# Kernel optimization log

Hardware: AMD Instinct MI355X
Metric: run time of the kernel (lower is better)

The kernel has to match this reference:

```python
import jax, jax.numpy as jnp
import numpy as np
import math

B, D_MODEL, EMB, ORDER, SEQ = 4, 64, 33, 64, 256
TARGET, FAST_PCT, SLOW_PCT = 0.01, 0.3, 1.5


def _pos_emb(L, emb_dim):
    # PositionalEmbedding: t in [0,1], complex exponential bands
    t = jnp.linspace(0.0, 1.0, L)[None, :, None]                     # [1,L,1]
    bands = (emb_dim - 1) // 2
    t_r = jnp.linspace(0.0, L - 1.0, L)[None, :, None]
    w = 2.0 * math.pi * t_r / L
    f = jnp.linspace(1e-4, bands - 1.0, bands)[None, None]
    zc = jnp.exp(-1j * f * w)
    z = jnp.concatenate([t, zc.real, zc.imag], axis=-1)              # [1,L,emb_dim]
    return z.astype(jnp.float32), t.astype(jnp.float32)


def setup_inputs() -> dict:
    key = jax.random.key(0)
    ks = jax.random.split(key, 24)
    z, _ = _pos_emb(SEQ, EMB)

    def lin(k, fan_in, fan_out):
        return jax.random.normal(k, (fan_in, fan_out), jnp.float32) / np.sqrt(fan_in)

    inp = {
        'x': jax.random.normal(ks[0], (B, D_MODEL, SEQ, SEQ), jnp.float32),
        'z': z,
        'Xw1': lin(ks[1], EMB, ORDER), 'Xb1': jax.random.normal(ks[2], (ORDER,), jnp.float32) * 0.02,
        'Xw2': lin(ks[3], ORDER, ORDER), 'Xb2': jax.random.normal(ks[4], (ORDER,), jnp.float32) * 0.02,
        'Xw3': lin(ks[5], ORDER, ORDER), 'Xb3': jax.random.normal(ks[6], (ORDER,), jnp.float32) * 0.02,
        'Xwo': lin(ks[7], ORDER, D_MODEL),
        'Xfreq': jnp.ones((1, ORDER), jnp.float32),  # Sin freq, w=1, shared across layers
        'Yw1': lin(ks[8], EMB, ORDER), 'Yb1': jax.random.normal(ks[9], (ORDER,), jnp.float32) * 0.02,
        'Yw2': lin(ks[10], ORDER, ORDER), 'Yb2': jax.random.normal(ks[11], (ORDER,), jnp.float32) * 0.02,
        'Yw3': lin(ks[12], ORDER, ORDER), 'Yb3': jax.random.normal(ks[13], (ORDER,), jnp.float32) * 0.02,
        'Ywo': lin(ks[14], ORDER, D_MODEL),
        'Yfreq': jnp.ones((1, ORDER), jnp.float32),
        'bias': jax.random.normal(ks[15], (D_MODEL,), jnp.float32),
        'L': SEQ,
    }
    return inp


def _implicit_filter(z, w1, b1, w2, b2, w3, b3, wo, freq, t, deltas):
    # MLP with shared Sin activation, then exponential modulation (shift=0)
    h = jnp.sin(freq * (z @ w1 + b1))
    h = jnp.sin(freq * (h @ w2 + b2))
    h = jnp.sin(freq * (h @ w3 + b3))
    h = h @ wo                                   # [1,L,d_model]
    decay = jnp.exp(-t * jnp.abs(deltas))        # [1,L,d_model]
    return h * decay


def reference(x, z, Xw1, Xb1, Xw2, Xb2, Xw3, Xb3, Xwo, Xfreq,
              Yw1, Yb1, Yw2, Yb2, Yw3, Yb3, Ywo, Yfreq, bias, L):
    d_model = x.shape[1]
    t = jnp.linspace(0.0, 1.0, L)[None, :, None].astype(jnp.float32)
    max_dec = math.log(TARGET) / FAST_PCT
    min_dec = math.log(TARGET) / SLOW_PCT
    deltas = jnp.linspace(min_dec, max_dec, d_model)[None, None].astype(jnp.float32)

    hx = _implicit_filter(z, Xw1, Xb1, Xw2, Xb2, Xw3, Xb3, Xwo, Xfreq, t, deltas)
    hy = _implicit_filter(z, Yw1, Yb1, Yw2, Yb2, Yw3, Yb3, Ywo, Yfreq, t, deltas)
    # separable outer-product 2D kernel: [1,L,L,d_model] -> [d_model,L,L]
    k = jnp.einsum('ijk,imk->ijmk', hx, hy)[0]
    k = jnp.transpose(k, (2, 0, 1))

    fft_size = 2 * L
    k_f = jnp.fft.rfft2(k, s=(fft_size, fft_size)) / fft_size       # [D, 2L, L+1]
    u_f = jnp.fft.rfft2(x.astype(jnp.float32), s=(fft_size, fft_size))  # [B, D, 2L, L+1]
    y = jnp.fft.irfft2(u_f * k_f, s=(fft_size, fft_size))[..., :L, :L]
    out = y + x * bias[:, None, None]
    return out.astype(x.dtype)
```

## Files before the change

### kernel.cpp

```cpp
#include <hip/hip_runtime.h>

#define SL 256

typedef _Float16 f16;
typedef _Float16 f16x8 __attribute__((ext_vector_type(8)));
typedef _Float16 f16x4 __attribute__((ext_vector_type(4)));
typedef float f32x4 __attribute__((ext_vector_type(4)));

__global__ __launch_bounds__(64) void k_filters(
    const float* __restrict__ z,
    const float* __restrict__ Xw1, const float* __restrict__ Xb1,
    const float* __restrict__ Xw2, const float* __restrict__ Xb2,
    const float* __restrict__ Xw3, const float* __restrict__ Xb3,
    const float* __restrict__ Xwo, const float* __restrict__ Xfreq,
    const float* __restrict__ Yw1, const float* __restrict__ Yb1,
    const float* __restrict__ Yw2, const float* __restrict__ Yb2,
    const float* __restrict__ Yw3, const float* __restrict__ Yb3,
    const float* __restrict__ Ywo, const float* __restrict__ Yfreq,
    f16* __restrict__ hxT, f16* __restrict__ hyT)
{
    const int l = blockIdx.x;
    const int sel = blockIdx.y;
    const int t = threadIdx.x;
    const float* w1 = sel ? Yw1 : Xw1;  const float* b1 = sel ? Yb1 : Xb1;
    const float* w2 = sel ? Yw2 : Xw2;  const float* b2 = sel ? Yb2 : Xb2;
    const float* w3 = sel ? Yw3 : Xw3;  const float* b3 = sel ? Yb3 : Xb3;
    const float* wo = sel ? Ywo : Xwo;  const float* freq = sel ? Yfreq : Xfreq;
    f16* hT = sel ? hyT : hxT;

    __shared__ float zb[33];
    __shared__ float ha[64];
    __shared__ float hb[64];

    if (t < 33) zb[t] = z[l * 33 + t];
    __syncthreads();

    const float fr = freq[t];
    float s = b1[t];
    for (int k = 0; k < 33; ++k) s += zb[k] * w1[k * 64 + t];
    ha[t] = sinf(fr * s);
    __syncthreads();

    s = b2[t];
    for (int k = 0; k < 64; ++k) s += ha[k] * w2[k * 64 + t];
    hb[t] = sinf(fr * s);
    __syncthreads();

    s = b3[t];
    for (int k = 0; k < 64; ++k) s += hb[k] * w3[k * 64 + t];
    ha[t] = sinf(fr * s);
    __syncthreads();

    s = 0.f;
    for (int k = 0; k < 64; ++k) s += ha[k] * wo[k * 64 + t];

    const float MIN_DEC = -3.0701134573253937f;
    const float MAX_DEC = -15.350567286626968f;
    float ad = fabsf(MIN_DEC + (MAX_DEC - MIN_DEC) * ((float)t / 63.0f));
    float tl = (float)l / 255.0f;
    hT[t * 256 + l] = (f16)(s * expf(-tl * ad));
}

__device__ __forceinline__ f16x8 cvt8(float4 a, float4 b)
{
    f16x8 h;
    h[0] = (f16)a.x; h[1] = (f16)a.y; h[2] = (f16)a.z; h[3] = (f16)a.w;
    h[4] = (f16)b.x; h[5] = (f16)b.y; h[6] = (f16)b.z; h[7] = (f16)b.w;
    return h;
}

__device__ __forceinline__ void build_R(f16* R, const f16* __restrict__ hc,
                                        int tid)
{
    for (int idx = tid; idx < 8 * 520; idx += 512) {
        int c = idx / 520;
        int k = idx - c * 520;
        int u = k + c;
        R[idx] = (u <= 255) ? hc[255 - u] : (f16)0.f;
    }
}

template<int J0>
__device__ __forceinline__ void phase1(
    const float* __restrict__ xr0, const float* __restrict__ xr1,
    const f16* __restrict__ R, f32x4 (&acc)[16], int ln, int quad)
{
    constexpr int QS = (J0 == 0) ? 4 : 8;
    float4 a0 = *(const float4*)xr0;
    float4 a1 = *(const float4*)(xr0 + 4);
    float4 b0 = *(const float4*)xr1;
    float4 b1 = *(const float4*)(xr1 + 4);

#pragma unroll
    for (int s = 0; s < QS; ++s) {
        const int q0 = s * 32;
        f16x8 af0 = cvt8(a0, a1);
        f16x8 af1 = cvt8(b0, b1);
        if (s + 1 < QS) {
            a0 = *(const float4*)(xr0 + q0 + 32);
            a1 = *(const float4*)(xr0 + q0 + 36);
            b0 = *(const float4*)(xr1 + q0 + 32);
            b1 = *(const float4*)(xr1 + q0 + 36);
        }
#pragma unroll
        for (int c8 = 0; c8 < 8; ++c8) {
            if (32 * s <= J0 + c8 * 16 + 15) {
                int j = J0 + c8 * 16 + ln;
                int s0 = 255 - j + q0 + quad * 8;
                int c = s0 & 7;
                f16x8 bf = *(const f16x8*)&R[c * 520 + (s0 - c)];
                acc[c8] = __builtin_amdgcn_mfma_f32_16x16x32_f16(
                    af0, bf, acc[c8], 0, 0, 0);
                acc[8 + c8] = __builtin_amdgcn_mfma_f32_16x16x32_f16(
                    af1, bf, acc[8 + c8], 0, 0, 0);
            }
        }
    }
}

__global__ __launch_bounds__(512, 4) void k_fused(
    const float* __restrict__ x, const f16* __restrict__ hxT,
    const f16* __restrict__ hyT, const float* __restrict__ bias,
    float* __restrict__ out)
{
    const int bd = blockIdx.x & 255;
    const int j0 = (blockIdx.x >> 8) << 7;
    const int d  = bd & 63;
    const int tid  = threadIdx.x;
    const int lane = tid & 63;
    const int wave = tid >> 6;
    const int ln   = lane & 15;
    const int quad = lane >> 4;

    __shared__ __align__(16) f16 tmp[128 * 256];
    __shared__ __align__(16) f16 R[8 * 520];

    const float* xbd = x + (size_t)bd * (SL * SL);

    build_R(R, hyT + d * 256, tid);

    f32x4 acc[16];
#pragma unroll
    for (int a = 0; a < 16; ++a) acc[a] = (f32x4){0.f, 0.f, 0.f, 0.f};

    __syncthreads();

    {
        const float* xr0 = xbd + (wave * 32 + ln) * SL + quad * 8;
        const float* xr1 = xr0 + 16 * SL;
        if (j0 == 0) phase1<0>(xr0, xr1, R, acc, ln, quad);
        else         phase1<128>(xr0, xr1, R, acc, ln, quad);

#pragma unroll
        for (int r = 0; r < 2; ++r)
#pragma unroll
            for (int c8 = 0; c8 < 8; ++c8) {
                int jl = c8 * 16 + ln;
                int pb = wave * 32 + r * 16 + quad * 4;
                f32x4 a = acc[r * 8 + c8];
                f16x4 v;
                v[0] = (f16)a[0]; v[1] = (f16)a[1];
                v[2] = (f16)a[2]; v[3] = (f16)a[3];
                *(f16x4*)&tmp[jl * 256 + (pb ^ ((jl & 7) << 3))] = v;
            }
    }

    __syncthreads();
    build_R(R, hxT + d * 256, tid);
#pragma unroll
    for (int a = 0; a < 16; ++a) acc[a] = (f32x4){0.f, 0.f, 0.f, 0.f};
    __syncthreads();

    const int igrp = wave & 3;
    const int jgrp = wave >> 2;
    const int nst = (igrp + 1) * 2;
    for (int s = 0; s < nst; ++s) {
        const int p0 = s * 32;
        f16x8 af[4];
#pragma unroll
        for (int rt = 0; rt < 4; ++rt) {
            int jl = jgrp * 64 + rt * 16 + ln;
            int off = (p0 + quad * 8) ^ ((jl & 7) << 3);
            af[rt] = *(const f16x8*)&tmp[jl * 256 + off];
        }
#pragma unroll
        for (int ct = 0; ct < 4; ++ct) {
            if (p0 <= igrp * 64 + ct * 16 + 15) {
                int i = igrp * 64 + ct * 16 + ln;
                int s0 = 255 - i + p0 + quad * 8;
                int c = s0 & 7;
                f16x8 bf = *(const f16x8*)&R[c * 520 + (s0 - c)];
#pragma unroll
                for (int rt = 0; rt < 4; ++rt)
                    acc[rt * 4 + ct] = __builtin_amdgcn_mfma_f32_16x16x32_f16(
                        af[rt], bf, acc[rt * 4 + ct], 0, 0, 0);
            }
        }
    }

    const float bv = bias[d];
    const float sc = 1.0f / 512.0f;
    float* obd = out + (size_t)bd * (SL * SL);
#pragma unroll
    for (int rt = 0; rt < 4; ++rt)
#pragma unroll
        for (int ct = 0; ct < 4; ++ct) {
            int i = igrp * 64 + ct * 16 + ln;
            int j = j0 + jgrp * 64 + rt * 16 + quad * 4;
            f32x4 a = acc[rt * 4 + ct];
            float4 xv = *(const float4*)(xbd + i * SL + j);
            float4 o;
            o.x = a[0] * sc + xv.x * bv;
            o.y = a[1] * sc + xv.y * bv;
            o.z = a[2] * sc + xv.z * bv;
            o.w = a[3] * sc + xv.w * bv;
            *(float4*)(obd + i * SL + j) = o;
        }
}

extern "C" void kernel_launch(void* const* d_in, const int* in_sizes, int n_in,
                              void* d_out, int out_size, void* d_ws, size_t ws_size,
                              hipStream_t stream)
{
    (void)in_sizes; (void)n_in; (void)out_size; (void)ws_size;
    const float* x     = (const float*)d_in[0];
    const float* z     = (const float*)d_in[1];
    const float* Xw1   = (const float*)d_in[2];
    const float* Xb1   = (const float*)d_in[3];
    const float* Xw2   = (const float*)d_in[4];
    const float* Xb2   = (const float*)d_in[5];
    const float* Xw3   = (const float*)d_in[6];
    const float* Xb3   = (const float*)d_in[7];
    const float* Xwo   = (const float*)d_in[8];
    const float* Xfreq = (const float*)d_in[9];
    const float* Yw1   = (const float*)d_in[10];
    const float* Yb1   = (const float*)d_in[11];
    const float* Yw2   = (const float*)d_in[12];
    const float* Yb2   = (const float*)d_in[13];
    const float* Yw3   = (const float*)d_in[14];
    const float* Yb3   = (const float*)d_in[15];
    const float* Ywo   = (const float*)d_in[16];
    const float* Yfreq = (const float*)d_in[17];
    const float* bias  = (const float*)d_in[18];

    f16* hxT = (f16*)d_ws;
    f16* hyT = hxT + 64 * 256;

    k_filters<<<dim3(256, 2), 64, 0, stream>>>(
        z, Xw1, Xb1, Xw2, Xb2, Xw3, Xb3, Xwo, Xfreq,
        Yw1, Yb1, Yw2, Yb2, Yw3, Yb3, Ywo, Yfreq, hxT, hyT);
    k_fused<<<512, 512, 0, stream>>>(x, hxT, hyT, bias, (float*)d_out);
}
```

Measured before the change: 169.8 us.

## Balance triangular causal-conv work across blocks and waves via interleaved tile mapping

```diff
diff --git a/kernel.cpp b/kernel.cpp
--- a/kernel.cpp
+++ b/kernel.cpp
@@ -80,12 +80,18 @@
     }
 }
 
-template<int J0>
+template<int H>
+__device__ __forceinline__ constexpr int jmap(int c8)
+{
+    return H ? 64 + c8 * 16 : (c8 < 4 ? c8 * 16 : 192 + (c8 - 4) * 16);
+}
+
+template<int H>
 __device__ __forceinline__ void phase1(
     const float* __restrict__ xr0, const float* __restrict__ xr1,
     const f16* __restrict__ R, f32x4 (&acc)[16], int ln, int quad)
 {
-    constexpr int QS = (J0 == 0) ? 4 : 8;
+    constexpr int QS = H ? 6 : 8;
     float4 a0 = *(const float4*)xr0;
     float4 a1 = *(const float4*)(xr0 + 4);
     float4 b0 = *(const float4*)xr1;
@@ -104,8 +110,8 @@
         }
 #pragma unroll
         for (int c8 = 0; c8 < 8; ++c8) {
-            if (32 * s <= J0 + c8 * 16 + 15) {
-                int j = J0 + c8 * 16 + ln;
+            if (32 * s <= jmap<H>(c8) + 15) {
+                int j = jmap<H>(c8) + ln;
                 int s0 = 255 - j + q0 + quad * 8;
                 int c = s0 & 7;
                 f16x8 bf = *(const f16x8*)&R[c * 520 + (s0 - c)];
@@ -124,7 +130,7 @@
     float* __restrict__ out)
 {
     const int bd = blockIdx.x & 255;
-    const int j0 = (blockIdx.x >> 8) << 7;
+    const int h  = blockIdx.x >> 8;
     const int d  = bd & 63;
     const int tid  = threadIdx.x;
     const int lane = tid & 63;
@@ -148,8 +154,8 @@
     {
         const float* xr0 = xbd + (wave * 32 + ln) * SL + quad * 8;
         const float* xr1 = xr0 + 16 * SL;
-        if (j0 == 0) phase1<0>(xr0, xr1, R, acc, ln, quad);
-        else         phase1<128>(xr0, xr1, R, acc, ln, quad);
+        if (h == 0) phase1<0>(xr0, xr1, R, acc, ln, quad);
+        else        phase1<1>(xr0, xr1, R, acc, ln, quad);
 
 #pragma unroll
         for (int r = 0; r < 2; ++r)
@@ -173,7 +179,7 @@
 
     const int igrp = wave & 3;
     const int jgrp = wave >> 2;
-    const int nst = (igrp + 1) * 2;
+    const int nst = ((192 + igrp * 16 + 15) >> 5) + 1;
     for (int s = 0; s < nst; ++s) {
         const int p0 = s * 32;
         f16x8 af[4];
@@ -185,8 +191,8 @@
         }
 #pragma unroll
         for (int ct = 0; ct < 4; ++ct) {
-            if (p0 <= igrp * 64 + ct * 16 + 15) {
-                int i = igrp * 64 + ct * 16 + ln;
+            if (p0 <= ct * 64 + igrp * 16 + 15) {
+                int i = ct * 64 + igrp * 16 + ln;
                 int s0 = 255 - i + p0 + quad * 8;
                 int c = s0 & 7;
                 f16x8 bf = *(const f16x8*)&R[c * 520 + (s0 - c)];
@@ -202,11 +208,13 @@
     const float sc = 1.0f / 512.0f;
     float* obd = out + (size_t)bd * (SL * SL);
 #pragma unroll
-    for (int rt = 0; rt < 4; ++rt)
+    for (int rt = 0; rt < 4; ++rt) {
+        int jt = jgrp * 4 + rt;
+        int jg = h ? 64 + jt * 16 : (jt < 4 ? jt * 16 : 192 + (jt - 4) * 16);
 #pragma unroll
         for (int ct = 0; ct < 4; ++ct) {
-            int i = igrp * 64 + ct * 16 + ln;
-            int j = j0 + jgrp * 64 + rt * 16 + quad * 4;
+            int i = ct * 64 + igrp * 16 + ln;
+            int j = jg + quad * 4;
             f32x4 a = acc[rt * 4 + ct];
             float4 xv = *(const float4*)(xbd + i * SL + j);
             float4 o;
@@ -216,6 +224,7 @@
             o.w = a[3] * sc + xv.w * bv;
             *(float4*)(obd + i * SL + j) = o;
         }
+    }
 }
 
 extern "C" void kernel_launch(void* const* d_in, const int* in_sizes, int n_in,
```

Measured after the change: 181.4 us. 1.07x slower.
